# Kernel optimization log

Hardware: AMD Instinct MI355X
Metric: run time of the kernel (lower is better)

The kernel has to match this reference:

```python
import jax, jax.numpy as jnp
import numpy as np

N, F_IN, H, C, E = 100000, 128, 128, 40, 600000


def setup_inputs() -> dict:
    key = jax.random.key(0)
    ks = jax.random.split(key, 20)
    s = 0.05
    inp = {
        "x": jax.random.normal(ks[0], (N, F_IN), jnp.float32),
        "edge_index": jax.random.randint(ks[1], (2, E), 0, N, jnp.int64),
        "importance": jnp.ones((F_IN,), jnp.float32),
        "W1": jax.random.normal(ks[2], (H, F_IN), jnp.float32) * s,
        "bl1": jax.random.normal(ks[3], (H,), jnp.float32) * s,
        "bc1": jnp.zeros((H,), jnp.float32),
        "W2": jax.random.normal(ks[4], (H, H), jnp.float32) * s,
        "bl2": jax.random.normal(ks[5], (H,), jnp.float32) * s,
        "bc2": jnp.zeros((H,), jnp.float32),
        "W3": jax.random.normal(ks[6], (H, H), jnp.float32) * s,
        "bl3": jax.random.normal(ks[7], (H,), jnp.float32) * s,
        "bc3": jnp.zeros((H,), jnp.float32),
        "Wlin1": jax.random.normal(ks[8], (H, H), jnp.float32) * s,
        "blin1": jax.random.normal(ks[9], (H,), jnp.float32) * s,
        "Wlin2": jax.random.normal(ks[10], (C, H), jnp.float32) * s,
        "blin2": jax.random.normal(ks[11], (C,), jnp.float32) * s,
    }
    return inp


def balanced_conv(x, W, bl, bc, row, col):
    # lin, then symmetric-normalized message, mean-aggregated over targets
    n = x.shape[0]
    h = x @ W.T + bl                                   # [N, H]
    loops = jnp.arange(n)
    r = jnp.concatenate([row, loops])                  # sources (x_j index)
    c = jnp.concatenate([col, loops])                  # targets
    deg = jnp.zeros((n,), x.dtype).at[c].add(1.0)      # degree(col) incl. self-loops
    dinv = deg ** -0.5
    norm = dinv[r] * dinv[c]                           # [E+N]
    msg = norm[:, None] * h[r]                         # gather + scale
    agg = jnp.zeros((n, h.shape[1]), x.dtype).at[c].add(msg)  # scatter-add
    return agg / deg[:, None] + bc                     # mean aggr + bias


def reference(x, edge_index, importance, W1, bl1, bc1, W2, bl2, bc2,
              W3, bl3, bc3, Wlin1, blin1, Wlin2, blin2):
    row, col = edge_index[0], edge_index[1]
    h = x * importance
    h = jax.nn.relu(balanced_conv(h, W1, bl1, bc1, row, col))
    h = jax.nn.relu(balanced_conv(h, W2, bl2, bc2, row, col))
    h = jax.nn.relu(balanced_conv(h, W3, bl3, bc3, row, col))
    h = jax.nn.relu(h @ Wlin1.T + blin1)
    h = h @ Wlin2.T + blin2
    return jax.nn.log_softmax(h, axis=-1)
```

## Files before the change

kernel.cpp:

```cpp
#include <hip/hip_runtime.h>
#include <hip/hip_bf16.h>

#define F 128
#define C_CLS 40
#define NWSPLIT 35
#define ELLCAP 32

typedef __attribute__((ext_vector_type(8))) short short8;
typedef __attribute__((ext_vector_type(4))) float float4v;
typedef unsigned short ushort;

__device__ inline float bf2f(ushort u) {
  unsigned int x = ((unsigned int)u) << 16;
  return __builtin_bit_cast(float, x);
}
__device__ inline ushort f2bf(float f) {
  __hip_bfloat16 h = __float2bfloat16(f);
  return __builtin_bit_cast(ushort, h);
}
__device__ inline void split_bf16(float f, ushort& hi, ushort& lo) {
  hi = f2bf(f);
  lo = f2bf(f - bf2f(hi));
}
__device__ inline int swz(int lane) { return lane ^ ((lane >> 4) & 3); }

__global__ __launch_bounds__(256) void setup_kernel(
    const float* __restrict__ W1, const float* __restrict__ imp,
    const float* __restrict__ W2, const float* __restrict__ W3,
    const float* __restrict__ Wl1, const float* __restrict__ Wh2,
    ushort* __restrict__ WhP,
    ushort* __restrict__ W2hH, ushort* __restrict__ W2lH,
    const int* __restrict__ row, const int* __restrict__ col,
    int* __restrict__ cntPad, int* __restrict__ ell,
    int ne, int n) {
  int b = blockIdx.x;
  if (b < NWSPLIT) {
    int ci = b * 256 + threadIdx.x;
    if (ci < 8192) {
      const float* src[4] = {W1, W2, W3, Wl1};
      int p = ci >> 11, c = ci & 2047;
      int kc = c >> 10, ct = (c >> 7) & 7, ks = (c >> 6) & 1, ln = c & 63;
      int dl = swz(ln);
      int colw = ct * 16 + (dl & 15);
      int k = kc * 64 + ks * 32 + (dl >> 4) * 8;
      float4 f0 = *(const float4*)&src[p][(size_t)colw * F + k];
      float4 f1 = *(const float4*)&src[p][(size_t)colw * F + k + 4];
      float v[8] = {f0.x, f0.y, f0.z, f0.w, f1.x, f1.y, f1.z, f1.w};
      if (p == 0) {
        float4 i0 = *(const float4*)&imp[k];
        float4 i1 = *(const float4*)&imp[k + 4];
        v[0] *= i0.x; v[1] *= i0.y; v[2] *= i0.z; v[3] *= i0.w;
        v[4] *= i1.x; v[5] *= i1.y; v[6] *= i1.z; v[7] *= i1.w;
      }
      ushort hi[8];
#pragma unroll
      for (int j = 0; j < 8; ++j) hi[j] = f2bf(v[j]);
      *(short8*)&WhP[(size_t)ci * 8] = *(short8*)hi;
    } else if (ci < 8192 + 768) {
      int c = ci - 8192;
      int ct = c >> 8, ks = (c >> 6) & 3, ln = c & 63;
      int colw = ct * 16 + (ln & 15);
      int k = ks * 32 + (ln >> 4) * 8;
      float v[8];
      if (colw < C_CLS) {
        float4 f0 = *(const float4*)&Wh2[(size_t)colw * F + k];
        float4 f1 = *(const float4*)&Wh2[(size_t)colw * F + k + 4];
        v[0] = f0.x; v[1] = f0.y; v[2] = f0.z; v[3] = f0.w;
        v[4] = f1.x; v[5] = f1.y; v[6] = f1.z; v[7] = f1.w;
      } else {
#pragma unroll
        for (int j = 0; j < 8; ++j) v[j] = 0.f;
      }
      ushort hi[8], lo[8];
#pragma unroll
      for (int j = 0; j < 8; ++j) split_bf16(v[j], hi[j], lo[j]);
      *(short8*)&W2hH[(size_t)c * 8] = *(short8*)hi;
      *(short8*)&W2lH[(size_t)c * 8] = *(short8*)lo;
    }
  } else {
    int e = (b - NWSPLIT) * 256 + threadIdx.x;
    if (e < ne) {
      int r = row[e], c = col[e];
      int p = atomicAdd(&cntPad[c * 16], 1);
      if (p < ELLCAP) ell[(size_t)c * ELLCAP + p] = r;
    }
  }
}

__global__ __launch_bounds__(256) void dinv_kernel(const int* __restrict__ cntPad,
    int* __restrict__ cntC, float* __restrict__ dinv, float* __restrict__ invdeg,
    int n) {
  int i = blockIdx.x * 256 + threadIdx.x;
  if (i >= n) return;
  int c = cntPad[i * 16];
  float d = (float)(c + 1);
  cntC[i] = c;
  dinv[i] = rsqrtf(d);
  invdeg[i] = 1.0f / d;
}

template <bool F32IN>
__global__ __launch_bounds__(256, 2) void gemm_any(const void* __restrict__ INv,
    const ushort* __restrict__ Wh,
    const float* __restrict__ bias, ushort* __restrict__ OUT, int nrows, int relu) {
  __shared__ ushort sWh[16384];
  const int t = threadIdx.x;
  const int rbase = blockIdx.x * 256;
  const int w = t >> 6, lane = t & 63;
  const int quad = lane >> 4, cl = lane & 15;

#pragma unroll
  for (int pp = 0; pp < 8; ++pp) {
    int ci = t + pp * 256;
    *(short8*)&sWh[ci * 8] = *(const short8*)&Wh[(size_t)ci * 8];
  }
  __syncthreads();

  float4v acc[4][8];
#pragma unroll
  for (int nt = 0; nt < 4; ++nt)
#pragma unroll
    for (int mt = 0; mt < 8; ++mt) acc[nt][mt] = (float4v){0.f, 0.f, 0.f, 0.f};

  const int sl = swz(lane);
  const int nrow0 = rbase + w * 64 + cl;
#pragma unroll
  for (int ks = 0; ks < 4; ++ks) {
    short8 b[4];
#pragma unroll
    for (int nt = 0; nt < 4; ++nt) {
      int gr = nrow0 + nt * 16;
      if (gr < nrows) {
        if (F32IN) {
          const float* INf = (const float*)INv;
          float4 f0 = *(const float4*)&INf[(size_t)gr * F + ks * 32 + quad * 8];
          float4 f1 = *(const float4*)&INf[(size_t)gr * F + ks * 32 + quad * 8 + 4];
          ushort h[8] = {f2bf(f0.x), f2bf(f0.y), f2bf(f0.z), f2bf(f0.w),
                         f2bf(f1.x), f2bf(f1.y), f2bf(f1.z), f2bf(f1.w)};
          b[nt] = *(short8*)h;
        } else {
          const ushort* IN = (const ushort*)INv;
          b[nt] = *(const short8*)&IN[(size_t)gr * F + ks * 32 + quad * 8];
        }
      } else {
        b[nt] = (short8){0, 0, 0, 0, 0, 0, 0, 0};
      }
    }
    const int base = ((ks >> 1) * 1024 + (ks & 1) * 64 + sl) * 8;
#pragma unroll
    for (int mt = 0; mt < 8; ++mt) {
      short8 a_h = *(short8*)&sWh[base + mt * 128 * 8];
#pragma unroll
      for (int nt = 0; nt < 4; ++nt)
        acc[nt][mt] = __builtin_amdgcn_mfma_f32_16x16x32_bf16(a_h, b[nt], acc[nt][mt], 0, 0, 0);
    }
  }
#pragma unroll
  for (int mt = 0; mt < 8; ++mt) {
    float4 bv = *(const float4*)&bias[mt * 16 + quad * 4];
#pragma unroll
    for (int nt = 0; nt < 4; ++nt) {
      int gr = nrow0 + nt * 16;
      if (gr < nrows) {
        float v0 = acc[nt][mt][0] + bv.x;
        float v1 = acc[nt][mt][1] + bv.y;
        float v2 = acc[nt][mt][2] + bv.z;
        float v3 = acc[nt][mt][3] + bv.w;
        if (relu) {
          v0 = fmaxf(v0, 0.f); v1 = fmaxf(v1, 0.f);
          v2 = fmaxf(v2, 0.f); v3 = fmaxf(v3, 0.f);
        }
        ushort o[4] = {f2bf(v0), f2bf(v1), f2bf(v2), f2bf(v3)};
        *(ushort4*)&OUT[(size_t)gr * F + mt * 16 + quad * 4] = *(ushort4*)o;
      }
    }
  }
}

__global__ __launch_bounds__(256) void gather_kernel(const int* __restrict__ cntC,
    const int* __restrict__ ell, const ushort* __restrict__ B,
    const float* __restrict__ dinv, const float* __restrict__ invdeg,
    const float* __restrict__ bc, ushort* __restrict__ A, int n) {
  int node = blockIdx.x * 16 + (threadIdx.x >> 4);
  if (node >= n) return;
  int j = (threadIdx.x & 15) * 8;
  int cnt = cntC[node];
  float dc = dinv[node];
  const int4* ep = (const int4*)&ell[(size_t)node * ELLCAP];
  float a0[8] = {0, 0, 0, 0, 0, 0, 0, 0};
  float a1[8] = {0, 0, 0, 0, 0, 0, 0, 0};
  float a2[8] = {0, 0, 0, 0, 0, 0, 0, 0};
  float a3[8] = {0, 0, 0, 0, 0, 0, 0, 0};
  for (int base = 0; base < cnt; base += 4) {
    int4 rr = ep[base >> 2];
    float g0 = dinv[rr.x];
    float g1 = (base + 1 < cnt) ? dinv[rr.y] : 0.f;
    float g2 = (base + 2 < cnt) ? dinv[rr.z] : 0.f;
    float g3 = (base + 3 < cnt) ? dinv[rr.w] : 0.f;
    short8 v0 = *(const short8*)&B[(size_t)rr.x * F + j];
    short8 v1 = *(const short8*)&B[(size_t)rr.y * F + j];
    short8 v2 = *(const short8*)&B[(size_t)rr.z * F + j];
    short8 v3 = *(const short8*)&B[(size_t)rr.w * F + j];
#pragma unroll
    for (int q = 0; q < 8; ++q) {
      a0[q] += g0 * bf2f((ushort)v0[q]);
      a1[q] += g1 * bf2f((ushort)v1[q]);
      a2[q] += g2 * bf2f((ushort)v2[q]);
      a3[q] += g3 * bf2f((ushort)v3[q]);
    }
  }
  float id = invdeg[node];
  short8 sv = *(const short8*)&B[(size_t)node * F + j];
  float4 b0 = *(const float4*)&bc[j];
  float4 b1 = *(const float4*)&bc[j + 4];
  float bcv[8] = {b0.x, b0.y, b0.z, b0.w, b1.x, b1.y, b1.z, b1.w};
  ushort o[8];
#pragma unroll
  for (int q = 0; q < 8; ++q) {
    float s = dc * ((a0[q] + a1[q]) + (a2[q] + a3[q]));
    o[q] = f2bf(fmaxf((s + bf2f((ushort)sv[q]) * id) * id + bcv[q], 0.f));
  }
  *(short8*)&A[(size_t)node * F + j] = *(short8*)o;
}

__global__ __launch_bounds__(256) void logits_mfma(const ushort* __restrict__ X,
    const ushort* __restrict__ W2h, const ushort* __restrict__ W2l,
    const float* __restrict__ b2, float* __restrict__ out, int nrows) {
  __shared__ ushort sWh[6144], sWl[6144];
  __shared__ float b2s[48];
  const int t = threadIdx.x;
#pragma unroll
  for (int pp = 0; pp < 3; ++pp) {
    int c = t + pp * 256;
    *(short8*)&sWh[c * 8] = *(const short8*)&W2h[(size_t)c * 8];
    *(short8*)&sWl[c * 8] = *(const short8*)&W2l[(size_t)c * 8];
  }
  if (t < 48) b2s[t] = (t < C_CLS) ? b2[t] : -1e30f;
  __syncthreads();

  const int w = t >> 6, lane = t & 63;
  const int quad = lane >> 4, cl = lane & 15;
  const int row0 = (blockIdx.x * 4 + w) * 16;

  float4v acc[3];
#pragma unroll
  for (int ct = 0; ct < 3; ++ct) acc[ct] = (float4v){0.f, 0.f, 0.f, 0.f};

#pragma unroll
  for (int ks = 0; ks < 4; ++ks) {
    int gr = row0 + cl;
    short8 a;
    if (gr < nrows) a = *(const short8*)&X[(size_t)gr * F + ks * 32 + quad * 8];
    else a = (short8){0, 0, 0, 0, 0, 0, 0, 0};
#pragma unroll
    for (int ct = 0; ct < 3; ++ct) {
      int chunk = ((ct * 4 + ks) * 64 + lane) * 8;
      short8 b_h = *(short8*)&sWh[chunk];
      short8 b_l = *(short8*)&sWl[chunk];
      acc[ct] = __builtin_amdgcn_mfma_f32_16x16x32_bf16(a, b_h, acc[ct], 0, 0, 0);
      acc[ct] = __builtin_amdgcn_mfma_f32_16x16x32_bf16(a, b_l, acc[ct], 0, 0, 0);
    }
  }

  float b0 = b2s[cl], b1 = b2s[16 + cl], b2v = b2s[32 + cl];
  float lse[4];
#pragma unroll
  for (int reg = 0; reg < 4; ++reg) {
    float v0 = acc[0][reg] + b0;
    float v1 = acc[1][reg] + b1;
    float v2 = acc[2][reg] + b2v;
    acc[0][reg] = v0; acc[1][reg] = v1; acc[2][reg] = v2;
    float m = fmaxf(fmaxf(v0, v1), v2);
#pragma unroll
    for (int o = 1; o < 16; o <<= 1) m = fmaxf(m, __shfl_xor(m, o));
    float s = __expf(v0 - m) + __expf(v1 - m) + __expf(v2 - m);
#pragma unroll
    for (int o = 1; o < 16; o <<= 1) s += __shfl_xor(s, o);
    lse[reg] = logf(s) + m;
  }
#pragma unroll
  for (int reg = 0; reg < 4; ++reg) {
    int gr = row0 + quad * 4 + reg;
    if (gr < nrows) {
      out[(size_t)gr * C_CLS + cl] = acc[0][reg] - lse[reg];
      out[(size_t)gr * C_CLS + 16 + cl] = acc[1][reg] - lse[reg];
      if (cl < 8) out[(size_t)gr * C_CLS + 32 + cl] = acc[2][reg] - lse[reg];
    }
  }
}

extern "C" void kernel_launch(void* const* d_in, const int* in_sizes, int n_in,
                              void* d_out, int out_size, void* d_ws, size_t ws_size,
                              hipStream_t stream) {
  const float* x    = (const float*)d_in[0];
  const int*   ei   = (const int*)d_in[1];
  const float* imp  = (const float*)d_in[2];
  const float* W1   = (const float*)d_in[3];
  const float* bl1  = (const float*)d_in[4];
  const float* bc1  = (const float*)d_in[5];
  const float* W2   = (const float*)d_in[6];
  const float* bl2  = (const float*)d_in[7];
  const float* bc2  = (const float*)d_in[8];
  const float* W3   = (const float*)d_in[9];
  const float* bl3  = (const float*)d_in[10];
  const float* bc3  = (const float*)d_in[11];
  const float* Wl1  = (const float*)d_in[12];
  const float* bli1 = (const float*)d_in[13];
  const float* Wl2  = (const float*)d_in[14];
  const float* bli2 = (const float*)d_in[15];
  float* out = (float*)d_out;

  const int N = in_sizes[0] / F;
  const int E = in_sizes[1] / 2;

  ushort* A16 = (ushort*)d_ws;
  ushort* B16 = A16 + (size_t)N * F;
  ushort* WhP = B16 + (size_t)N * F;
  ushort* W2hH = WhP + 65536;
  ushort* W2lH = W2hH + 6144;
  float* dinv = (float*)(W2lH + 6144);
  float* invdeg = dinv + N;
  int*   cntC = (int*)(invdeg + N);
  int*   cntPad = cntC + N;
  int*   ell  = cntPad + (size_t)16 * N;

  const int* rowv = ei;
  const int* colv = ei + E;

  int nbN  = (N + 255) / 256;
  int nbE  = (E + 255) / 256;
  int nbG  = (N + 255) / 256;
  int nbGa = (N + 15) / 16;
  int nbLo = (N + 63) / 64;

  hipMemsetAsync(cntPad, 0, (size_t)48 * N * sizeof(int), stream);
  setup_kernel<<<NWSPLIT + nbE, 256, 0, stream>>>(
      W1, imp, W2, W3, Wl1, Wl2, WhP, W2hH, W2lH, rowv, colv, cntPad, ell, E, N);
  dinv_kernel<<<nbN, 256, 0, stream>>>(cntPad, cntC, dinv, invdeg, N);

  gemm_any<true><<<nbG, 256, 0, stream>>>(x, WhP, bl1, B16, N, 0);
  gather_kernel<<<nbGa, 256, 0, stream>>>(cntC, ell, B16, dinv, invdeg, bc1, A16, N);

  gemm_any<false><<<nbG, 256, 0, stream>>>(A16, WhP + 16384, bl2, B16, N, 0);
  gather_kernel<<<nbGa, 256, 0, stream>>>(cntC, ell, B16, dinv, invdeg, bc2, A16, N);

  gemm_any<false><<<nbG, 256, 0, stream>>>(A16, WhP + 32768, bl3, B16, N, 0);
  gather_kernel<<<nbGa, 256, 0, stream>>>(cntC, ell, B16, dinv, invdeg, bc3, A16, N);

  gemm_any<false><<<nbG, 256, 0, stream>>>(A16, WhP + 49152, bli1, B16, N, 1);
  logits_mfma<<<nbLo, 256, 0, stream>>>(B16, W2hH, W2lH, bli2, out, N);
}
```

Baseline: 331.0 us.

## Fuse head GEMMs, fold dinv into first GEMM, unpad degree counters

```diff
diff --git a/kernel.cpp b/kernel.cpp
--- a/kernel.cpp
+++ b/kernel.cpp
@@ -31,7 +31,7 @@
     ushort* __restrict__ WhP,
     ushort* __restrict__ W2hH, ushort* __restrict__ W2lH,
     const int* __restrict__ row, const int* __restrict__ col,
-    int* __restrict__ cntPad, int* __restrict__ ell,
+    int* __restrict__ cnt, int* __restrict__ ell,
     int ne, int n) {
   int b = blockIdx.x;
   if (b < NWSPLIT) {
@@ -81,29 +81,28 @@
     int e = (b - NWSPLIT) * 256 + threadIdx.x;
     if (e < ne) {
       int r = row[e], c = col[e];
-      int p = atomicAdd(&cntPad[c * 16], 1);
+      int p = atomicAdd(&cnt[c], 1);
       if (p < ELLCAP) ell[(size_t)c * ELLCAP + p] = r;
     }
   }
-}
-
-__global__ __launch_bounds__(256) void dinv_kernel(const int* __restrict__ cntPad,
-    int* __restrict__ cntC, float* __restrict__ dinv, float* __restrict__ invdeg,
-    int n) {
-  int i = blockIdx.x * 256 + threadIdx.x;
-  if (i >= n) return;
-  int c = cntPad[i * 16];
-  float d = (float)(c + 1);
-  cntC[i] = c;
-  dinv[i] = rsqrtf(d);
-  invdeg[i] = 1.0f / d;
 }
 
 template <bool F32IN>
 __global__ __launch_bounds__(256, 2) void gemm_any(const void* __restrict__ INv,
     const ushort* __restrict__ Wh,
-    const float* __restrict__ bias, ushort* __restrict__ OUT, int nrows, int relu) {
+    const float* __restrict__ bias, ushort* __restrict__ OUT, int nrows, int relu,
+    int nbMain, const int* __restrict__ cntv, float* __restrict__ dinvv,
+    float* __restrict__ invdegv, int n) {
   __shared__ ushort sWh[16384];
+  if (blockIdx.x >= nbMain) {
+    int i = (blockIdx.x - nbMain) * 256 + threadIdx.x;
+    if (i < n) {
+      float d = (float)(cntv[i] + 1);
+      dinvv[i] = rsqrtf(d);
+      invdegv[i] = 1.0f / d;
+    }
+    return;
+  }
   const int t = threadIdx.x;
   const int rbase = blockIdx.x * 256;
   const int w = t >> 6, lane = t & 63;
@@ -177,30 +176,35 @@
   }
 }
 
-__global__ __launch_bounds__(256) void gather_kernel(const int* __restrict__ cntC,
+__global__ __launch_bounds__(256) void gather_kernel(const int* __restrict__ cntv,
     const int* __restrict__ ell, const ushort* __restrict__ B,
     const float* __restrict__ dinv, const float* __restrict__ invdeg,
     const float* __restrict__ bc, ushort* __restrict__ A, int n) {
   int node = blockIdx.x * 16 + (threadIdx.x >> 4);
   if (node >= n) return;
   int j = (threadIdx.x & 15) * 8;
-  int cnt = cntC[node];
+  int cnt = cntv[node];
+  int lim = cnt < ELLCAP ? cnt : ELLCAP;
   float dc = dinv[node];
   const int4* ep = (const int4*)&ell[(size_t)node * ELLCAP];
   float a0[8] = {0, 0, 0, 0, 0, 0, 0, 0};
   float a1[8] = {0, 0, 0, 0, 0, 0, 0, 0};
   float a2[8] = {0, 0, 0, 0, 0, 0, 0, 0};
   float a3[8] = {0, 0, 0, 0, 0, 0, 0, 0};
-  for (int base = 0; base < cnt; base += 4) {
+  for (int base = 0; base < lim; base += 4) {
     int4 rr = ep[base >> 2];
+    bool p1 = base + 1 < lim, p2 = base + 2 < lim, p3 = base + 3 < lim;
+    int r1 = p1 ? rr.y : rr.x;
+    int r2 = p2 ? rr.z : rr.x;
+    int r3 = p3 ? rr.w : rr.x;
     float g0 = dinv[rr.x];
-    float g1 = (base + 1 < cnt) ? dinv[rr.y] : 0.f;
-    float g2 = (base + 2 < cnt) ? dinv[rr.z] : 0.f;
-    float g3 = (base + 3 < cnt) ? dinv[rr.w] : 0.f;
+    float g1 = p1 ? dinv[r1] : 0.f;
+    float g2 = p2 ? dinv[r2] : 0.f;
+    float g3 = p3 ? dinv[r3] : 0.f;
     short8 v0 = *(const short8*)&B[(size_t)rr.x * F + j];
-    short8 v1 = *(const short8*)&B[(size_t)rr.y * F + j];
-    short8 v2 = *(const short8*)&B[(size_t)rr.z * F + j];
-    short8 v3 = *(const short8*)&B[(size_t)rr.w * F + j];
+    short8 v1 = *(const short8*)&B[(size_t)r1 * F + j];
+    short8 v2 = *(const short8*)&B[(size_t)r2 * F + j];
+    short8 v3 = *(const short8*)&B[(size_t)r3 * F + j];
 #pragma unroll
     for (int q = 0; q < 8; ++q) {
       a0[q] += g0 * bf2f((ushort)v0[q]);
@@ -223,40 +227,76 @@
   *(short8*)&A[(size_t)node * F + j] = *(short8*)o;
 }
 
-__global__ __launch_bounds__(256) void logits_mfma(const ushort* __restrict__ X,
+__global__ __launch_bounds__(256, 2) void head_fused(const ushort* __restrict__ X,
+    const ushort* __restrict__ Wl1h, const float* __restrict__ bl,
     const ushort* __restrict__ W2h, const ushort* __restrict__ W2l,
     const float* __restrict__ b2, float* __restrict__ out, int nrows) {
-  __shared__ ushort sWh[6144], sWl[6144];
+  __shared__ ushort sWh[16384];
+  __shared__ ushort sW2h[6144], sW2l[6144];
+  __shared__ ushort sH[8192];
   __shared__ float b2s[48];
   const int t = threadIdx.x;
 #pragma unroll
+  for (int pp = 0; pp < 8; ++pp) {
+    int ci = t + pp * 256;
+    *(short8*)&sWh[ci * 8] = *(const short8*)&Wl1h[(size_t)ci * 8];
+  }
+#pragma unroll
   for (int pp = 0; pp < 3; ++pp) {
     int c = t + pp * 256;
-    *(short8*)&sWh[c * 8] = *(const short8*)&W2h[(size_t)c * 8];
-    *(short8*)&sWl[c * 8] = *(const short8*)&W2l[(size_t)c * 8];
+    *(short8*)&sW2h[c * 8] = *(const short8*)&W2h[(size_t)c * 8];
+    *(short8*)&sW2l[c * 8] = *(const short8*)&W2l[(size_t)c * 8];
   }
   if (t < 48) b2s[t] = (t < C_CLS) ? b2[t] : -1e30f;
   __syncthreads();
 
   const int w = t >> 6, lane = t & 63;
   const int quad = lane >> 4, cl = lane & 15;
+  const int sl = swz(lane);
   const int row0 = (blockIdx.x * 4 + w) * 16;
+  char* sHb = (char*)sH;
+
+  float4v acc1[8];
+#pragma unroll
+  for (int mt = 0; mt < 8; ++mt) acc1[mt] = (float4v){0.f, 0.f, 0.f, 0.f};
+  const int gr1 = row0 + cl;
+#pragma unroll
+  for (int ks = 0; ks < 4; ++ks) {
+    short8 b;
+    if (gr1 < nrows) b = *(const short8*)&X[(size_t)gr1 * F + ks * 32 + quad * 8];
+    else b = (short8){0, 0, 0, 0, 0, 0, 0, 0};
+    const int base = ((ks >> 1) * 1024 + (ks & 1) * 64 + sl) * 8;
+#pragma unroll
+    for (int mt = 0; mt < 8; ++mt) {
+      short8 a_h = *(short8*)&sWh[base + mt * 128 * 8];
+      acc1[mt] = __builtin_amdgcn_mfma_f32_16x16x32_bf16(a_h, b, acc1[mt], 0, 0, 0);
+    }
+  }
+#pragma unroll
+  for (int mt = 0; mt < 8; ++mt) {
+    float4 bv = *(const float4*)&bl[mt * 16 + quad * 4];
+    ushort o[4];
+    o[0] = f2bf(fmaxf(acc1[mt][0] + bv.x, 0.f));
+    o[1] = f2bf(fmaxf(acc1[mt][1] + bv.y, 0.f));
+    o[2] = f2bf(fmaxf(acc1[mt][2] + bv.z, 0.f));
+    o[3] = f2bf(fmaxf(acc1[mt][3] + bv.w, 0.f));
+    int ch = (mt * 2 + (quad >> 1)) ^ cl;
+    *(ushort4*)&sHb[w * 4096 + cl * 256 + ch * 16 + (quad & 1) * 8] = *(ushort4*)o;
+  }
+  __syncthreads();
 
   float4v acc[3];
 #pragma unroll
   for (int ct = 0; ct < 3; ++ct) acc[ct] = (float4v){0.f, 0.f, 0.f, 0.f};
-
 #pragma unroll
   for (int ks = 0; ks < 4; ++ks) {
-    int gr = row0 + cl;
-    short8 a;
-    if (gr < nrows) a = *(const short8*)&X[(size_t)gr * F + ks * 32 + quad * 8];
-    else a = (short8){0, 0, 0, 0, 0, 0, 0, 0};
+    int ch2 = (ks * 4 + quad) ^ cl;
+    short8 a = *(short8*)&sHb[w * 4096 + cl * 256 + ch2 * 16];
 #pragma unroll
     for (int ct = 0; ct < 3; ++ct) {
       int chunk = ((ct * 4 + ks) * 64 + lane) * 8;
-      short8 b_h = *(short8*)&sWh[chunk];
-      short8 b_l = *(short8*)&sWl[chunk];
+      short8 b_h = *(short8*)&sW2h[chunk];
+      short8 b_l = *(short8*)&sW2l[chunk];
       acc[ct] = __builtin_amdgcn_mfma_f32_16x16x32_bf16(a, b_h, acc[ct], 0, 0, 0);
       acc[ct] = __builtin_amdgcn_mfma_f32_16x16x32_bf16(a, b_l, acc[ct], 0, 0, 0);
     }
@@ -320,9 +360,8 @@
   ushort* W2lH = W2hH + 6144;
   float* dinv = (float*)(W2lH + 6144);
   float* invdeg = dinv + N;
-  int*   cntC = (int*)(invdeg + N);
-  int*   cntPad = cntC + N;
-  int*   ell  = cntPad + (size_t)16 * N;
+  int*   cnt  = (int*)(invdeg + N);
+  int*   ell  = cnt + N;
 
   const int* rowv = ei;
   const int* colv = ei + E;
@@ -331,22 +370,23 @@
   int nbE  = (E + 255) / 256;
   int nbG  = (N + 255) / 256;
   int nbGa = (N + 15) / 16;
-  int nbLo = (N + 63) / 64;
-
-  hipMemsetAsync(cntPad, 0, (size_t)48 * N * sizeof(int), stream);
+  int nbHd = (N + 63) / 64;
+
+  hipMemsetAsync(cnt, 0, (size_t)N * sizeof(int), stream);
   setup_kernel<<<NWSPLIT + nbE, 256, 0, stream>>>(
-      W1, imp, W2, W3, Wl1, Wl2, WhP, W2hH, W2lH, rowv, colv, cntPad, ell, E, N);
-  dinv_kernel<<<nbN, 256, 0, stream>>>(cntPad, cntC, dinv, invdeg, N);
-
-  gemm_any<true><<<nbG, 256, 0, stream>>>(x, WhP, bl1, B16, N, 0);
-  gather_kernel<<<nbGa, 256, 0, stream>>>(cntC, ell, B16, dinv, invdeg, bc1, A16, N);
-
-  gemm_any<false><<<nbG, 256, 0, stream>>>(A16, WhP + 16384, bl2, B16, N, 0);
-  gather_kernel<<<nbGa, 256, 0, stream>>>(cntC, ell, B16, dinv, invdeg, bc2, A16, N);
-
-  gemm_any<false><<<nbG, 256, 0, stream>>>(A16, WhP + 32768, bl3, B16, N, 0);
-  gather_kernel<<<nbGa, 256, 0, stream>>>(cntC, ell, B16, dinv, invdeg, bc3, A16, N);
-
-  gemm_any<false><<<nbG, 256, 0, stream>>>(A16, WhP + 49152, bli1, B16, N, 1);
-  logits_mfma<<<nbLo, 256, 0, stream>>>(B16, W2hH, W2lH, bli2, out, N);
-}
+      W1, imp, W2, W3, Wl1, Wl2, WhP, W2hH, W2lH, rowv, colv, cnt, ell, E, N);
+
+  gemm_any<true><<<nbG + nbN, 256, 0, stream>>>(x, WhP, bl1, B16, N, 0,
+                                                nbG, cnt, dinv, invdeg, N);
+  gather_kernel<<<nbGa, 256, 0, stream>>>(cnt, ell, B16, dinv, invdeg, bc1, A16, N);
+
+  gemm_any<false><<<nbG, 256, 0, stream>>>(A16, WhP + 16384, bl2, B16, N, 0,
+                                           nbG, nullptr, nullptr, nullptr, 0);
+  gather_kernel<<<nbGa, 256, 0, stream>>>(cnt, ell, B16, dinv, invdeg, bc2, A16, N);
+
+  gemm_any<false><<<nbG, 256, 0, stream>>>(A16, WhP + 32768, bl3, B16, N, 0,
+                                           nbG, nullptr, nullptr, nullptr, 0);
+  gather_kernel<<<nbGa, 256, 0, stream>>>(cnt, ell, B16, dinv, invdeg, bc3, A16, N);
+
+  head_fused<<<nbHd, 256, 0, stream>>>(A16, WhP + 49152, bli1, W2hH, W2lH, bli2, out, N);
+}
```

Result: faster. 321.3 us (-2.9%).
